# Optimization experiments

Hardware: AMD Instinct MI355X
Metric: run time of the kernel (lower is better)

Reference implementation:

```python
import jax, jax.numpy as jnp
import numpy as np

N_NODES = 100000
N_EDGES = 1250000
D = 64
K = 5
EPS = 1e-8


def setup_inputs() -> dict:
    key = jax.random.key(0)
    k1, k2, k3, k4 = jax.random.split(key, 4)
    x = jax.random.normal(k1, (N_NODES, D), dtype=jnp.float32)
    mask = jax.random.normal(k2, (N_NODES, 1), dtype=jnp.float32)
    edge_index = jax.random.randint(k3, (2, N_EDGES), 0, N_NODES, dtype=jnp.int64)
    # orthogonal-ish init for the linear layer (QR of gaussian), gain for tanh = 5/3
    g = jax.random.normal(k4, (D, D), dtype=jnp.float32)
    q, _ = jnp.linalg.qr(g)
    W = (5.0 / 3.0) * q.astype(jnp.float32)
    b = jnp.zeros((D,), dtype=jnp.float32)
    alpha = jnp.float32(0.001)
    return {"x": x, "mask": mask, "edge_index": edge_index, "W": W, "b": b, "alpha": alpha}


def _forward(x, mask, edge_index, W, b, alpha):
    n = x.shape[0]
    # x_fn: Linear + Tanh
    h = jnp.tanh(x @ W.T + b)  # [N, D]
    src = edge_index[0]
    dst = edge_index[1]
    hs = h[src]  # [E, D] gather
    hd = h[dst]  # [E, D] gather
    # torch cosine_similarity with eps clamp on each norm
    ns = jnp.maximum(jnp.sqrt(jnp.sum(hs * hs, axis=-1)), EPS)
    nd = jnp.maximum(jnp.sqrt(jnp.sum(hd * hd, axis=-1)), EPS)
    cos = jnp.sum(hs * hd, axis=-1) / (ns * nd)
    edge_weights = jax.nn.relu(cos)  # [E]

    # gcn_norm with self loops (PyG APPNP default): D^-1/2 (A + I) D^-1/2
    loop = jnp.arange(n, dtype=src.dtype)
    row = jnp.concatenate([src, loop])
    col = jnp.concatenate([dst, loop])
    w = jnp.concatenate([edge_weights, jnp.ones((n,), dtype=edge_weights.dtype)])
    deg = jax.ops.segment_sum(w, col, num_segments=n)
    dis = jnp.where(deg > 0, jax.lax.rsqrt(jnp.maximum(deg, EPS)), 0.0)
    norm_w = dis[row] * w * dis[col]  # [E + N]

    # APPNP: K steps of f = (1-alpha) * A_hat @ f + alpha * f0
    f0 = jax.nn.relu(mask)  # [N, 1]
    f = f0
    for _ in range(K):
        msg = norm_w[:, None] * f[row]  # gather + weight
        agg = jax.ops.segment_sum(msg, col, num_segments=n)  # scatter-add
        f = (1.0 - alpha) * agg + alpha * f0
    return f, edge_weights


def reference(x, mask, edge_index, W, b, alpha):
    return _forward(x, mask, edge_index, W, b, alpha)
```

## Files before the change

### kernel.cpp

```cpp
#include <hip/hip_runtime.h>
#include <hip/hip_fp16.h>
#include <math.h>

#define N_NODES 100000
#define N_EDGES 1250000
#define D 64
#define EPS 1e-8f

#define ZERO_BLOCKS 391
#define GEMM_BLOCKS 1024
#define RANK_BLOCKS 4883
#define NODE_BLOCKS 391

__global__ __launch_bounds__(256) void k_gemm_zero(
    const float* __restrict__ x, const float* __restrict__ W,
    const float* __restrict__ b, __half* __restrict__ hn, int* __restrict__ cnt)
{
    if (blockIdx.x < ZERO_BLOCKS) {
        int i = blockIdx.x * 256 + threadIdx.x;
        if (i < N_NODES) cnt[i] = 0;
        return;
    }
    __shared__ float xrow[4][72];
    const int lane = threadIdx.x & 63;
    const int wid  = threadIdx.x >> 6;

    float Wreg[64];
    const float4* Wv = (const float4*)(W + lane * D);
    #pragma unroll
    for (int q = 0; q < 16; ++q) {
        float4 w4 = Wv[q];
        Wreg[4*q+0] = w4.x; Wreg[4*q+1] = w4.y;
        Wreg[4*q+2] = w4.z; Wreg[4*q+3] = w4.w;
    }
    const float bj = b[lane];
    float* xl = xrow[wid];

    const int wave   = (blockIdx.x - ZERO_BLOCKS) * 4 + wid;
    const int nwaves = GEMM_BLOCKS * 4;

    for (int row = wave; row < N_NODES; row += nwaves) {
        float xv = x[(size_t)row * D + lane];
        xl[lane] = xv;
        float acc = bj;
        #pragma unroll
        for (int q = 0; q < 16; ++q) {
            float4 xk4 = *(const float4*)(xl + 4*q);
            acc = fmaf(xk4.x, Wreg[4*q+0], acc);
            acc = fmaf(xk4.y, Wreg[4*q+1], acc);
            acc = fmaf(xk4.z, Wreg[4*q+2], acc);
            acc = fmaf(xk4.w, Wreg[4*q+3], acc);
        }
        float h = tanhf(acc);
        float s = h * h;
        #pragma unroll
        for (int m = 32; m >= 1; m >>= 1) s += __shfl_xor(s, m, 64);
        float nrm = fmaxf(sqrtf(s), EPS);
        hn[(size_t)row * D + lane] = __float2half_rn(h / nrm);
    }
}

__device__ __forceinline__ float dot8h(float4 a, float4 c)
{
    const __half2* ah = (const __half2*)&a;
    const __half2* ch = (const __half2*)&c;
    float p = 0.0f;
    #pragma unroll
    for (int q = 0; q < 4; ++q) {
        float2 af = __half22float2(ah[q]);
        float2 cf = __half22float2(ch[q]);
        p = fmaf(af.x, cf.x, p);
        p = fmaf(af.y, cf.y, p);
    }
    return p;
}

__global__ __launch_bounds__(256) void k_rank_cos(
    const int* __restrict__ ei, int* __restrict__ cnt, int* __restrict__ rank,
    const __half* __restrict__ hn, float* __restrict__ wout)
{
    const int b = blockIdx.x;
    const int r = b % 3;
    if (r == 0) {
        int e = (b / 3) * 256 + threadIdx.x;
        if (e < N_EDGES) {
            int d = ei[N_EDGES + e];
            rank[e] = atomicAdd(cnt + d, 1);
        }
        return;
    }
    int cb = (b / 3) * 2 + (r - 1);
    int t = cb * 256 + threadIdx.x;
    int g = t >> 3, sub = t & 7;
    if (g >= N_EDGES / 4) return;
    int e0 = g * 4;
    int4 ss = *(const int4*)(ei + e0);
    int4 dd = *(const int4*)(ei + N_EDGES + e0);

    float4 a0 = ((const float4*)(hn + (size_t)ss.x * D))[sub];
    float4 c0 = ((const float4*)(hn + (size_t)dd.x * D))[sub];
    float4 a1 = ((const float4*)(hn + (size_t)ss.y * D))[sub];
    float4 c1 = ((const float4*)(hn + (size_t)dd.y * D))[sub];
    float4 a2 = ((const float4*)(hn + (size_t)ss.z * D))[sub];
    float4 c2 = ((const float4*)(hn + (size_t)dd.z * D))[sub];
    float4 a3 = ((const float4*)(hn + (size_t)ss.w * D))[sub];
    float4 c3 = ((const float4*)(hn + (size_t)dd.w * D))[sub];

    float p0 = dot8h(a0, c0);
    float p1 = dot8h(a1, c1);
    float p2 = dot8h(a2, c2);
    float p3 = dot8h(a3, c3);
    p0 += __shfl_xor(p0, 1, 64);  p1 += __shfl_xor(p1, 1, 64);
    p2 += __shfl_xor(p2, 1, 64);  p3 += __shfl_xor(p3, 1, 64);
    p0 += __shfl_xor(p0, 2, 64);  p1 += __shfl_xor(p1, 2, 64);
    p2 += __shfl_xor(p2, 2, 64);  p3 += __shfl_xor(p3, 2, 64);
    p0 += __shfl_xor(p0, 4, 64);  p1 += __shfl_xor(p1, 4, 64);
    p2 += __shfl_xor(p2, 4, 64);  p3 += __shfl_xor(p3, 4, 64);

    if (sub == 0) {
        *(float4*)(wout + e0) = make_float4(
            fmaxf(p0, 0.0f), fmaxf(p1, 0.0f), fmaxf(p2, 0.0f), fmaxf(p3, 0.0f));
    }
}

__device__ __forceinline__ int wave_iscan(int v, int lane)
{
    int incl = v;
    #pragma unroll
    for (int m = 1; m < 64; m <<= 1) {
        int o = __shfl_up(incl, m, 64);
        if (lane >= m) incl += o;
    }
    return incl;
}

__global__ __launch_bounds__(256) void k_scan1(
    const int* __restrict__ cnt, int* __restrict__ rowptr, int* __restrict__ bsum)
{
    __shared__ int wsum[4];
    int t = threadIdx.x, b = blockIdx.x;
    int i = b * 256 + t;
    int lane = t & 63, wid = t >> 6;
    int v = (i < N_NODES) ? cnt[i] : 0;
    int incl = wave_iscan(v, lane);
    if (lane == 63) wsum[wid] = incl;
    __syncthreads();
    int off = 0;
    #pragma unroll
    for (int k = 0; k < 4; ++k) if (k < wid) off += wsum[k];
    if (i < N_NODES) rowptr[i] = off + incl - v;
    if (t == 255) bsum[b] = off + incl;
}

__global__ __launch_bounds__(512) void k_scan2(
    const int* __restrict__ bsum, int* __restrict__ boff, int nblk,
    int* __restrict__ rowptr)
{
    __shared__ int wsum[8];
    int t = threadIdx.x;
    int lane = t & 63, wid = t >> 6;
    int v = (t < nblk) ? bsum[t] : 0;
    int incl = wave_iscan(v, lane);
    if (lane == 63) wsum[wid] = incl;
    __syncthreads();
    int off = 0;
    #pragma unroll
    for (int k = 0; k < 8; ++k) if (k < wid) off += wsum[k];
    if (t < nblk) boff[t] = off + incl - v;
    if (t == 0) rowptr[N_NODES] = N_EDGES;
}

__global__ __launch_bounds__(256) void k_place(
    const int* __restrict__ ei, const int* __restrict__ rank_pos,
    const int* __restrict__ rowptr, const int* __restrict__ boff,
    const float* __restrict__ wsrc, int2* __restrict__ pairs)
{
    int e = blockIdx.x * 256 + threadIdx.x;
    if (e >= N_EDGES) return;
    int s = ei[e];
    int d = ei[N_EDGES + e];
    int pos = rowptr[d] + boff[d >> 8] + rank_pos[e];
    pairs[pos] = make_int2(s, __float_as_int(wsrc[e]));
}

__global__ __launch_bounds__(256) void k_dis_y(
    const int* __restrict__ rowptr, const int* __restrict__ boff,
    const int2* __restrict__ pairs, const float* __restrict__ mask,
    float* __restrict__ dis, float* __restrict__ y)
{
    int t = blockIdx.x * 256 + threadIdx.x;
    int node = t >> 3, l = t & 7;
    if (node >= N_NODES) return;
    int beg = rowptr[node] + boff[node >> 8];
    int np1 = node + 1;
    int end = rowptr[np1] + (np1 < N_NODES ? boff[np1 >> 8] : 0);
    float s = 0.0f;
    for (int j = beg + l; j < end; j += 8)
        s += __int_as_float(pairs[j].y);
    s += __shfl_xor(s, 1, 64);
    s += __shfl_xor(s, 2, 64);
    s += __shfl_xor(s, 4, 64);
    if (l == 0) {
        float di = rsqrtf(fmaxf(s + 1.0f, EPS));
        dis[node] = di;
        y[node] = di * fmaxf(mask[node], 0.0f);
    }
}

__global__ __launch_bounds__(256) void k_spmv(
    const int* __restrict__ rowptr, const int* __restrict__ boff,
    const int2* __restrict__ pairs,
    const float* __restrict__ y_in, const float* __restrict__ dis,
    const float* __restrict__ mask, const float* __restrict__ alpha_p,
    float* __restrict__ y_out, float* __restrict__ f_out)
{
    int t = blockIdx.x * 256 + threadIdx.x;
    int node = t >> 3, l = t & 7;
    if (node >= N_NODES) return;
    int beg = rowptr[node] + boff[node >> 8];
    int np1 = node + 1;
    int end = rowptr[np1] + (np1 < N_NODES ? boff[np1 >> 8] : 0);
    float sum = 0.0f;
    for (int j = beg + l; j < end; j += 8) {
        int2 p = pairs[j];
        sum += __int_as_float(p.y) * y_in[p.x];
    }
    sum += __shfl_xor(sum, 1, 64);
    sum += __shfl_xor(sum, 2, 64);
    sum += __shfl_xor(sum, 4, 64);
    if (l == 0) {
        float di = dis[node];
        float alpha = alpha_p[0];
        float f0 = fmaxf(mask[node], 0.0f);
        float fn = (1.0f - alpha) * di * (sum + y_in[node]) + alpha * f0;
        f_out[node] = fn;
        y_out[node] = di * fn;
    }
}

extern "C" void kernel_launch(void* const* d_in, const int* in_sizes, int n_in,
                              void* d_out, int out_size, void* d_ws, size_t ws_size,
                              hipStream_t stream)
{
    const float* x     = (const float*)d_in[0];
    const float* mask  = (const float*)d_in[1];
    const int*   ei    = (const int*)  d_in[2];
    const float* W     = (const float*)d_in[3];
    const float* b     = (const float*)d_in[4];
    const float* alpha = (const float*)d_in[5];

    float* out_f = (float*)d_out;
    float* out_w = (float*)d_out + N_NODES;

    float* ws = (float*)d_ws;
    __half* hn     = (__half*)ws;
    int2*  pairs   = (int2*) (ws + 3200000);
    int*   rank    = (int*)  (ws + 5700000);
    int*   cnt     = (int*)  (ws + 6950000);
    int*   rowptr  = (int*)  (ws + 7050000);
    float* dis     =          ws + 7150016;
    float* y_a     =          ws + 7250016;
    float* y_b     =          ws + 7350016;
    float* f_scr   =          ws + 7450016;
    int*   bsum    = (int*)  (ws + 7550016);
    int*   boff    = (int*)  (ws + 7550528);

    const int edgeBlocks = (N_EDGES + 255) / 256;
    const int segBlocks  = (int)(((long long)N_NODES * 8 + 255) / 256);

    k_gemm_zero<<<ZERO_BLOCKS + GEMM_BLOCKS, 256, 0, stream>>>(x, W, b, hn, cnt);
    k_rank_cos<<<3 * RANK_BLOCKS, 256, 0, stream>>>(ei, cnt, rank, hn, out_w);
    k_scan1<<<NODE_BLOCKS, 256, 0, stream>>>(cnt, rowptr, bsum);
    k_scan2<<<1, 512, 0, stream>>>(bsum, boff, NODE_BLOCKS, rowptr);
    k_place<<<edgeBlocks, 256, 0, stream>>>(ei, rank, rowptr, boff, out_w, pairs);
    k_dis_y<<<segBlocks, 256, 0, stream>>>(rowptr, boff, pairs, mask, dis, y_a);

    k_spmv<<<segBlocks, 256, 0, stream>>>(rowptr, boff, pairs, y_a, dis, mask, alpha, y_b, f_scr);
    k_spmv<<<segBlocks, 256, 0, stream>>>(rowptr, boff, pairs, y_b, dis, mask, alpha, y_a, f_scr);
    k_spmv<<<segBlocks, 256, 0, stream>>>(rowptr, boff, pairs, y_a, dis, mask, alpha, y_b, f_scr);
    k_spmv<<<segBlocks, 256, 0, stream>>>(rowptr, boff, pairs, y_b, dis, mask, alpha, y_a, f_scr);
    k_spmv<<<segBlocks, 256, 0, stream>>>(rowptr, boff, pairs, y_a, dis, mask, alpha, y_b, out_f);
}
```

Baseline: 248.0 us.

## Drop zero-weight edges from CSR by ranking only positive-cosine edges

The cosine kernel now assigns per-destination ranks only to edges whose ReLU'd weight is positive, so edges with zero weight are excluded from the CSR. Placement skips them and the row end pointer comes from the scan total instead of the fixed edge count. With random features about half the edges are zero, which is meant to shrink the pair array that the degree pass and all five SpMV iterations read, and to halve the atomic counting. The cost is that atomics now wait on the gather-and-dot result instead of running in separate interleaved blocks.

Result: faster. 209.7 us (-15.4%).

```diff
diff --git a/kernel.cpp b/kernel.cpp
--- a/kernel.cpp
+++ b/kernel.cpp
@@ -9,8 +9,8 @@
 
 #define ZERO_BLOCKS 391
 #define GEMM_BLOCKS 1024
-#define RANK_BLOCKS 4883
 #define NODE_BLOCKS 391
+#define COSR_BLOCKS 9766
 
 __global__ __launch_bounds__(256) void k_gemm_zero(
     const float* __restrict__ x, const float* __restrict__ W,
@@ -75,22 +75,11 @@
     return p;
 }
 
-__global__ __launch_bounds__(256) void k_rank_cos(
-    const int* __restrict__ ei, int* __restrict__ cnt, int* __restrict__ rank,
-    const __half* __restrict__ hn, float* __restrict__ wout)
-{
-    const int b = blockIdx.x;
-    const int r = b % 3;
-    if (r == 0) {
-        int e = (b / 3) * 256 + threadIdx.x;
-        if (e < N_EDGES) {
-            int d = ei[N_EDGES + e];
-            rank[e] = atomicAdd(cnt + d, 1);
-        }
-        return;
-    }
-    int cb = (b / 3) * 2 + (r - 1);
-    int t = cb * 256 + threadIdx.x;
+__global__ __launch_bounds__(256) void k_cos_rank(
+    const int* __restrict__ ei, const __half* __restrict__ hn,
+    int* __restrict__ cnt, int* __restrict__ rank, float* __restrict__ wout)
+{
+    int t = blockIdx.x * 256 + threadIdx.x;
     int g = t >> 3, sub = t & 7;
     if (g >= N_EDGES / 4) return;
     int e0 = g * 4;
@@ -117,9 +106,19 @@
     p0 += __shfl_xor(p0, 4, 64);  p1 += __shfl_xor(p1, 4, 64);
     p2 += __shfl_xor(p2, 4, 64);  p3 += __shfl_xor(p3, 4, 64);
 
+    float w0 = fmaxf(p0, 0.0f);
+    float w1 = fmaxf(p1, 0.0f);
+    float w2 = fmaxf(p2, 0.0f);
+    float w3 = fmaxf(p3, 0.0f);
+
     if (sub == 0) {
-        *(float4*)(wout + e0) = make_float4(
-            fmaxf(p0, 0.0f), fmaxf(p1, 0.0f), fmaxf(p2, 0.0f), fmaxf(p3, 0.0f));
+        *(float4*)(wout + e0) = make_float4(w0, w1, w2, w3);
+    }
+    if (sub < 4) {
+        float w = (sub == 0) ? w0 : (sub == 1) ? w1 : (sub == 2) ? w2 : w3;
+        int   d = (sub == 0) ? dd.x : (sub == 1) ? dd.y : (sub == 2) ? dd.z : dd.w;
+        int   r = (w > 0.0f) ? atomicAdd(cnt + d, 1) : -1;
+        rank[e0 + sub] = r;
     }
 }
 
@@ -167,7 +166,7 @@
     #pragma unroll
     for (int k = 0; k < 8; ++k) if (k < wid) off += wsum[k];
     if (t < nblk) boff[t] = off + incl - v;
-    if (t == 0) rowptr[N_NODES] = N_EDGES;
+    if (t == nblk - 1) rowptr[N_NODES] = off + incl;
 }
 
 __global__ __launch_bounds__(256) void k_place(
@@ -177,10 +176,12 @@
 {
     int e = blockIdx.x * 256 + threadIdx.x;
     if (e >= N_EDGES) return;
+    float w = wsrc[e];
+    if (!(w > 0.0f)) return;
     int s = ei[e];
     int d = ei[N_EDGES + e];
     int pos = rowptr[d] + boff[d >> 8] + rank_pos[e];
-    pairs[pos] = make_int2(s, __float_as_int(wsrc[e]));
+    pairs[pos] = make_int2(s, __float_as_int(w));
 }
 
 __global__ __launch_bounds__(256) void k_dis_y(
@@ -269,7 +270,7 @@
     const int segBlocks  = (int)(((long long)N_NODES * 8 + 255) / 256);
 
     k_gemm_zero<<<ZERO_BLOCKS + GEMM_BLOCKS, 256, 0, stream>>>(x, W, b, hn, cnt);
-    k_rank_cos<<<3 * RANK_BLOCKS, 256, 0, stream>>>(ei, cnt, rank, hn, out_w);
+    k_cos_rank<<<COSR_BLOCKS, 256, 0, stream>>>(ei, hn, cnt, rank, out_w);
     k_scan1<<<NODE_BLOCKS, 256, 0, stream>>>(cnt, rowptr, bsum);
     k_scan2<<<1, 512, 0, stream>>>(bsum, boff, NODE_BLOCKS, rowptr);
     k_place<<<edgeBlocks, 256, 0, stream>>>(ei, rank, rowptr, boff, out_w, pairs);
```
